# Performance work log

Hardware: AMD Instinct MI355X
Metric: run time of the kernel (lower is better)

The kernel has to match this reference:

```python
import jax, jax.numpy as jnp
import numpy as np

N = 50000   # nodes
E = 600000  # edges
D = 128     # in/out features


def setup_inputs() -> dict:
    key = jax.random.key(0)
    k1, k2, k3, k4, k5, k6 = jax.random.split(key, 6)
    input = jax.random.normal(k1, (N, D), dtype=jnp.float32)
    W = jax.random.normal(k2, (D, D), dtype=jnp.float32) * (1.0 / np.sqrt(D))
    b = jax.random.normal(k3, (D,), dtype=jnp.float32) * 0.01
    adj_row = jnp.sort(jax.random.randint(k4, (E,), 0, N, dtype=jnp.int32))
    adj_col = jax.random.randint(k5, (E,), 0, N, dtype=jnp.int32)
    adj_val = jax.random.uniform(k6, (E,), dtype=jnp.float32)
    return {"input": input, "W": W, "b": b,
            "adj_row": adj_row, "adj_col": adj_col, "adj_val": adj_val}


def reference(input, W, b, adj_row, adj_col, adj_val):
    # support = Linear(input)  -> [N, D]
    support = jnp.einsum('nd,od->no', input, W) + b
    # sparse adj (COO) @ support : gather source rows, scale by edge value,
    # scatter-add into destination rows.
    msgs = support[adj_col] * adj_val[:, None]           # [E, D]
    agg = jax.ops.segment_sum(msgs, adj_row, num_segments=input.shape[0])
    return jnp.tanh(agg)
```

## Files before the change

### kernel.cpp

```cpp
#include <hip/hip_runtime.h>
#include <hip/hip_fp16.h>
#include <cmath>

#define DF 128
#define WPITCHH 136

typedef _Float16 f16x8 __attribute__((ext_vector_type(8)));
typedef _Float16 f16x4 __attribute__((ext_vector_type(4)));
typedef float    f32x4 __attribute__((ext_vector_type(4)));

__global__ __launch_bounds__(256)
void gemm_mfma_kernel(const float* __restrict__ X, const _Float16* __restrict__ Wh,
                      const float* __restrict__ bias, __half* __restrict__ S,
                      int N)
{
    __shared__ _Float16 Wl[DF * WPITCHH];

    const int t    = threadIdx.x;
    const int lane = t & 63;
    const int l15  = lane & 15;
    const int q    = lane >> 4;
    const int m0   = (blockIdx.x * 4 + (t >> 6)) * 16;

    #pragma unroll
    for (int l = 0; l < 8; ++l) {
        int flat = l * 256 + t;
        int r    = flat >> 4;
        int c8   = (flat & 15) * 8;
        f16x8 v = *(const f16x8*)(Wh + (size_t)r * DF + c8);
        *(f16x8*)(Wl + r * WPITCHH + c8) = v;
    }
    __syncthreads();
    if (m0 >= N) return;

    f32x4 acc[8];
    #pragma unroll
    for (int nt = 0; nt < 8; ++nt) acc[nt] = (f32x4){0.f, 0.f, 0.f, 0.f};

    const int xrow = min(m0 + l15, N - 1);
    #pragma unroll
    for (int kc = 0; kc < DF; kc += 32) {
        const float* xp = X + (size_t)xrow * DF + kc + q * 8;
        float4 xa = *(const float4*)xp;
        float4 xb = *(const float4*)(xp + 4);
        f16x8 A;
        A[0] = (_Float16)xa.x; A[1] = (_Float16)xa.y;
        A[2] = (_Float16)xa.z; A[3] = (_Float16)xa.w;
        A[4] = (_Float16)xb.x; A[5] = (_Float16)xb.y;
        A[6] = (_Float16)xb.z; A[7] = (_Float16)xb.w;
        #pragma unroll
        for (int nt = 0; nt < 8; ++nt) {
            f16x8 B = *(const f16x8*)(Wl + (nt * 16 + l15) * WPITCHH + kc + q * 8);
            acc[nt] = __builtin_amdgcn_mfma_f32_16x16x32_f16(B, A, acc[nt], 0, 0, 0);
        }
    }

    const int mrow = m0 + l15;
    if (mrow < N) {
        _Float16* rowp = (_Float16*)S + (size_t)mrow * DF;
        #pragma unroll
        for (int nt = 0; nt < 8; ++nt) {
            float4 bv = *(const float4*)(bias + nt * 16 + q * 4);
            f16x4 hv;
            hv[0] = (_Float16)(acc[nt][0] + bv.x);
            hv[1] = (_Float16)(acc[nt][1] + bv.y);
            hv[2] = (_Float16)(acc[nt][2] + bv.z);
            hv[3] = (_Float16)(acc[nt][3] + bv.w);
            *(f16x4*)(rowp + nt * 16 + q * 4) = hv;
        }
    }
}

__global__ __launch_bounds__(256)
void build_meta_kernel(const int* __restrict__ arow, const int* __restrict__ acol,
                       const float* __restrict__ aval, const float* __restrict__ W,
                       int* __restrict__ rowptr, int2* __restrict__ pk,
                       _Float16* __restrict__ Wh, int N, int E)
{
    int e = blockIdx.x * 256 + threadIdx.x;
    if (e >= E) return;
    if (e < DF * DF) Wh[e] = (_Float16)W[e];
    pk[e] = make_int2(acol[e] << 8, __float_as_int(aval[e]));
    int r = arow[e];
    int rprev = (e == 0) ? -1 : arow[e - 1];
    for (int n = rprev + 1; n <= r; ++n) rowptr[n] = e;
    if (e == E - 1) {
        for (int n = r + 1; n <= N; ++n) rowptr[n] = E;
    }
}

__global__ __launch_bounds__(256)
void agg_tanh_kernel(const __half* __restrict__ S, const int* __restrict__ rowptr,
                     const int2* __restrict__ pk, float* __restrict__ out, int Nn)
{
    const int n  = (blockIdx.x * 256 + threadIdx.x) >> 4;
    if (n >= Nn) return;
    const int f  = threadIdx.x & 15;
    const int fb = f * 16;

    const int start = rowptr[n];
    const int end   = rowptr[n + 1];
    const char* Sb  = (const char*)S;

    float acc[8];
    #pragma unroll
    for (int i = 0; i < 8; ++i) acc[i] = 0.f;

    for (int e = start; e < end; e += 4) {
        int2 p0 = pk[e];
        int2 p1 = (e + 1 < end) ? pk[e + 1] : make_int2(0, 0);
        int2 p2 = (e + 2 < end) ? pk[e + 2] : make_int2(0, 0);
        int2 p3 = (e + 3 < end) ? pk[e + 3] : make_int2(0, 0);
        f16x8 h0 = *(const f16x8*)(Sb + (size_t)(unsigned)p0.x + fb);
        f16x8 h1 = *(const f16x8*)(Sb + (size_t)(unsigned)p1.x + fb);
        f16x8 h2 = *(const f16x8*)(Sb + (size_t)(unsigned)p2.x + fb);
        f16x8 h3 = *(const f16x8*)(Sb + (size_t)(unsigned)p3.x + fb);
        const float v0 = __int_as_float(p0.y);
        const float v1 = __int_as_float(p1.y);
        const float v2 = __int_as_float(p2.y);
        const float v3 = __int_as_float(p3.y);
        #pragma unroll
        for (int i = 0; i < 8; ++i) {
            acc[i] += (float)h0[i] * v0 + (float)h1[i] * v1
                    + (float)h2[i] * v2 + (float)h3[i] * v3;
        }
    }

    float4 o0, o1;
    o0.x = tanhf(acc[0]); o0.y = tanhf(acc[1]);
    o0.z = tanhf(acc[2]); o0.w = tanhf(acc[3]);
    o1.x = tanhf(acc[4]); o1.y = tanhf(acc[5]);
    o1.z = tanhf(acc[6]); o1.w = tanhf(acc[7]);
    float* op = out + (size_t)n * DF + f * 8;
    *(float4*)op       = o0;
    *(float4*)(op + 4) = o1;
}

extern "C" void kernel_launch(void* const* d_in, const int* in_sizes, int n_in,
                              void* d_out, int out_size, void* d_ws, size_t ws_size,
                              hipStream_t stream)
{
    const float* X    = (const float*)d_in[0];
    const float* W    = (const float*)d_in[1];
    const float* bias = (const float*)d_in[2];
    const int*   arow = (const int*)  d_in[3];
    const int*   acol = (const int*)  d_in[4];
    const float* aval = (const float*)d_in[5];
    float* out = (float*)d_out;

    const int N = in_sizes[0] / DF;
    const int E = in_sizes[3];

    __half*   S      = (__half*)d_ws;
    _Float16* Wh     = (_Float16*)((char*)d_ws + (size_t)N * DF * sizeof(__half));
    int*      rowptr = (int*)((char*)Wh + (size_t)DF * DF * sizeof(_Float16));
    int2*     pk     = (int2*)(rowptr + (N + 2));

    build_meta_kernel<<<(E + 255) / 256, 256, 0, stream>>>(arow, acol, aval, W,
                                                           rowptr, pk, Wh, N, E);

    gemm_mfma_kernel<<<(N + 63) / 64, 256, 0, stream>>>(X, Wh, bias, S, N);

    agg_tanh_kernel<<<(N * 16 + 255) / 256, 256, 0, stream>>>(S, rowptr, pk, out, N);
}
```

Measured before the change: 123.5 us.

## Fuse metadata build into GEMM kernel and split edges across lanes in aggregation

Merges the CSR/packed-edge construction into the GEMM kernel as a grid-stride loop and converts W to fp16 directly while staging it in shared memory. This removes one kernel launch and the intermediate fp16 weight buffer. The aggregation kernel now gives each node a full 64-lane wavefront: groups of four lanes split the edges, and partial sums are combined with xor shuffles before each lane writes two tanh outputs. The aim is more memory-level parallelism on the gathers, at the cost of four times as many threads and extra shuffle work.

```diff
diff --git a/kernel.cpp b/kernel.cpp
--- a/kernel.cpp
+++ b/kernel.cpp
@@ -10,27 +10,49 @@
 typedef float    f32x4 __attribute__((ext_vector_type(4)));
 
 __global__ __launch_bounds__(256)
-void gemm_mfma_kernel(const float* __restrict__ X, const _Float16* __restrict__ Wh,
+void gemm_meta_kernel(const float* __restrict__ X, const float* __restrict__ W,
                       const float* __restrict__ bias, __half* __restrict__ S,
-                      int N)
+                      const int* __restrict__ arow, const int* __restrict__ acol,
+                      const float* __restrict__ aval,
+                      int* __restrict__ rowptr, int2* __restrict__ pk,
+                      int N, int E, int nthreads)
 {
     __shared__ _Float16 Wl[DF * WPITCHH];
 
-    const int t    = threadIdx.x;
-    const int lane = t & 63;
-    const int l15  = lane & 15;
-    const int q    = lane >> 4;
-    const int m0   = (blockIdx.x * 4 + (t >> 6)) * 16;
+    const int t   = threadIdx.x;
+    const int tid = blockIdx.x * 256 + t;
+
+    for (int e = tid; e < E; e += nthreads) {
+        pk[e] = make_int2(acol[e] << 8, __float_as_int(aval[e]));
+        int r     = arow[e];
+        int rprev = (e == 0) ? -1 : arow[e - 1];
+        for (int n = rprev + 1; n <= r; ++n) rowptr[n] = e;
+        if (e == E - 1) {
+            for (int n = r + 1; n <= N; ++n) rowptr[n] = E;
+        }
+    }
 
     #pragma unroll
     for (int l = 0; l < 8; ++l) {
         int flat = l * 256 + t;
         int r    = flat >> 4;
         int c8   = (flat & 15) * 8;
-        f16x8 v = *(const f16x8*)(Wh + (size_t)r * DF + c8);
+        const float* wp = W + (size_t)r * DF + c8;
+        float4 wa = *(const float4*)wp;
+        float4 wb = *(const float4*)(wp + 4);
+        f16x8 v;
+        v[0] = (_Float16)wa.x; v[1] = (_Float16)wa.y;
+        v[2] = (_Float16)wa.z; v[3] = (_Float16)wa.w;
+        v[4] = (_Float16)wb.x; v[5] = (_Float16)wb.y;
+        v[6] = (_Float16)wb.z; v[7] = (_Float16)wb.w;
         *(f16x8*)(Wl + r * WPITCHH + c8) = v;
     }
     __syncthreads();
+
+    const int lane = t & 63;
+    const int l15  = lane & 15;
+    const int q    = lane >> 4;
+    const int m0   = (blockIdx.x * 4 + (t >> 6)) * 16;
     if (m0 >= N) return;
 
     f32x4 acc[8];
@@ -72,31 +94,15 @@
 }
 
 __global__ __launch_bounds__(256)
-void build_meta_kernel(const int* __restrict__ arow, const int* __restrict__ acol,
-                       const float* __restrict__ aval, const float* __restrict__ W,
-                       int* __restrict__ rowptr, int2* __restrict__ pk,
-                       _Float16* __restrict__ Wh, int N, int E)
-{
-    int e = blockIdx.x * 256 + threadIdx.x;
-    if (e >= E) return;
-    if (e < DF * DF) Wh[e] = (_Float16)W[e];
-    pk[e] = make_int2(acol[e] << 8, __float_as_int(aval[e]));
-    int r = arow[e];
-    int rprev = (e == 0) ? -1 : arow[e - 1];
-    for (int n = rprev + 1; n <= r; ++n) rowptr[n] = e;
-    if (e == E - 1) {
-        for (int n = r + 1; n <= N; ++n) rowptr[n] = E;
-    }
-}
-
-__global__ __launch_bounds__(256)
 void agg_tanh_kernel(const __half* __restrict__ S, const int* __restrict__ rowptr,
                      const int2* __restrict__ pk, float* __restrict__ out, int Nn)
 {
-    const int n  = (blockIdx.x * 256 + threadIdx.x) >> 4;
+    const int n = (blockIdx.x * 256 + threadIdx.x) >> 6;
     if (n >= Nn) return;
-    const int f  = threadIdx.x & 15;
-    const int fb = f * 16;
+    const int lane = threadIdx.x & 63;
+    const int es   = lane & 3;
+    const int f    = lane >> 2;
+    const int fb   = f * 16;
 
     const int start = rowptr[n];
     const int end   = rowptr[n + 1];
@@ -106,34 +112,42 @@
     #pragma unroll
     for (int i = 0; i < 8; ++i) acc[i] = 0.f;
 
-    for (int e = start; e < end; e += 4) {
-        int2 p0 = pk[e];
-        int2 p1 = (e + 1 < end) ? pk[e + 1] : make_int2(0, 0);
-        int2 p2 = (e + 2 < end) ? pk[e + 2] : make_int2(0, 0);
-        int2 p3 = (e + 3 < end) ? pk[e + 3] : make_int2(0, 0);
-        f16x8 h0 = *(const f16x8*)(Sb + (size_t)(unsigned)p0.x + fb);
-        f16x8 h1 = *(const f16x8*)(Sb + (size_t)(unsigned)p1.x + fb);
-        f16x8 h2 = *(const f16x8*)(Sb + (size_t)(unsigned)p2.x + fb);
-        f16x8 h3 = *(const f16x8*)(Sb + (size_t)(unsigned)p3.x + fb);
-        const float v0 = __int_as_float(p0.y);
-        const float v1 = __int_as_float(p1.y);
-        const float v2 = __int_as_float(p2.y);
-        const float v3 = __int_as_float(p3.y);
-        #pragma unroll
-        for (int i = 0; i < 8; ++i) {
-            acc[i] += (float)h0[i] * v0 + (float)h1[i] * v1
-                    + (float)h2[i] * v2 + (float)h3[i] * v3;
+    for (int e = start; e < end; e += 8) {
+        const int ea = e + es;
+        int2 pa = (ea < end) ? pk[ea] : make_int2(0, 0);
+        f16x8 ha = *(const f16x8*)(Sb + (size_t)(unsigned)pa.x + fb);
+        const float va = __int_as_float(pa.y);
+        if (e + 4 < end) {
+            const int eb = ea + 4;
+            int2 pb = (eb < end) ? pk[eb] : make_int2(0, 0);
+            f16x8 hb = *(const f16x8*)(Sb + (size_t)(unsigned)pb.x + fb);
+            const float vb = __int_as_float(pb.y);
+            #pragma unroll
+            for (int i = 0; i < 8; ++i)
+                acc[i] += (float)ha[i] * va + (float)hb[i] * vb;
+        } else {
+            #pragma unroll
+            for (int i = 0; i < 8; ++i)
+                acc[i] += (float)ha[i] * va;
         }
     }
 
-    float4 o0, o1;
-    o0.x = tanhf(acc[0]); o0.y = tanhf(acc[1]);
-    o0.z = tanhf(acc[2]); o0.w = tanhf(acc[3]);
-    o1.x = tanhf(acc[4]); o1.y = tanhf(acc[5]);
-    o1.z = tanhf(acc[6]); o1.w = tanhf(acc[7]);
-    float* op = out + (size_t)n * DF + f * 8;
-    *(float4*)op       = o0;
-    *(float4*)(op + 4) = o1;
+    #pragma unroll
+    for (int i = 0; i < 8; ++i) {
+        acc[i] += __shfl_xor(acc[i], 1, 64);
+        acc[i] += __shfl_xor(acc[i], 2, 64);
+    }
+
+    float a0, a1;
+    if      (es == 0) { a0 = acc[0]; a1 = acc[1]; }
+    else if (es == 1) { a0 = acc[2]; a1 = acc[3]; }
+    else if (es == 2) { a0 = acc[4]; a1 = acc[5]; }
+    else              { a0 = acc[6]; a1 = acc[7]; }
+
+    float2 o;
+    o.x = tanhf(a0);
+    o.y = tanhf(a1);
+    *(float2*)(out + (size_t)n * DF + lane * 2) = o;
 }
 
 extern "C" void kernel_launch(void* const* d_in, const int* in_sizes, int n_in,
@@ -151,15 +165,15 @@
     const int N = in_sizes[0] / DF;
     const int E = in_sizes[3];
 
-    __half*   S      = (__half*)d_ws;
-    _Float16* Wh     = (_Float16*)((char*)d_ws + (size_t)N * DF * sizeof(__half));
-    int*      rowptr = (int*)((char*)Wh + (size_t)DF * DF * sizeof(_Float16));
-    int2*     pk     = (int2*)(rowptr + (N + 2));
+    __half* S      = (__half*)d_ws;
+    int*    rowptr = (int*)((char*)d_ws + (size_t)N * DF * sizeof(__half));
+    int2*   pk     = (int2*)(rowptr + (N + 2));
 
-    build_meta_kernel<<<(E + 255) / 256, 256, 0, stream>>>(arow, acol, aval, W,
-                                                           rowptr, pk, Wh, N, E);
+    const int gemmBlocks = (N + 63) / 64;
+    gemm_meta_kernel<<<gemmBlocks, 256, 0, stream>>>(X, W, bias, S,
+                                                     arow, acol, aval,
+                                                     rowptr, pk, N, E,
+                                                     gemmBlocks * 256);
 
-    gemm_mfma_kernel<<<(N + 63) / 64, 256, 0, stream>>>(X, Wh, bias, S, N);
-
-    agg_tanh_kernel<<<(N * 16 + 255) / 256, 256, 0, stream>>>(S, rowptr, pk, out, N);
+    agg_tanh_kernel<<<(N * 64 + 255) / 256, 256, 0, stream>>>(S, rowptr, pk, out, N);
 }
```

Measured after the change: 132.0 us. 1.07x slower.
